# Optimization experiments

Hardware: AMD Instinct MI355X
Metric: run time of the kernel (lower is better)

## Reference

```python
import jax, jax.numpy as jnp
import numpy as np

N_NODES = 50000
N_EDGES = 800000
D_IN = 256
D_OUT = 128
EPS = 1e-9


def setup_inputs() -> dict:
    key = jax.random.key(0)
    ks = jax.random.split(key, 6)
    feat = jax.random.normal(ks[0], (N_NODES, D_IN), dtype=jnp.float32)
    edge_row = jax.random.randint(ks[1], (N_EDGES,), 0, N_NODES)
    edge_col = jax.random.randint(ks[2], (N_EDGES,), 0, N_NODES)
    # normalized adjacency values (positive, ~1/degree scale)
    edge_val = jax.random.uniform(ks[3], (N_EDGES,), dtype=jnp.float32) / 16.0
    # xavier_uniform for Linear(dim_in, dim_out) weights, stored as [D_IN, D_OUT]
    limit = float(np.sqrt(6.0 / (D_IN + D_OUT)))
    W0 = jax.random.uniform(ks[4], (D_IN, D_OUT), minval=-limit, maxval=limit, dtype=jnp.float32)
    W1 = jax.random.uniform(ks[5], (D_IN, D_OUT), minval=-limit, maxval=limit, dtype=jnp.float32)
    zeros = jnp.zeros((D_OUT,), dtype=jnp.float32)
    ones = jnp.ones((D_OUT,), dtype=jnp.float32)
    return {
        "feat": feat,
        "W0": W0, "b0": zeros, "scale0": ones, "offset0": zeros,
        "W1": W1, "b1": zeros, "scale1": ones, "offset1": zeros,
        "edge_row": edge_row, "edge_col": edge_col, "edge_val": edge_val,
    }


def _spmm(edge_row, edge_col, edge_val, x):
    # out[r] += val * x[c] for each edge (r, c, val)  -- sparse adj @ x
    msgs = edge_val[:, None] * x[edge_col]  # [E, D]
    return jax.ops.segment_sum(msgs, edge_row, num_segments=N_NODES)


def _feat_trans(x, W, b, scale, offset):
    h = jax.nn.relu(x @ W + b)  # [N, D_OUT]
    mean = jnp.mean(h, axis=1, keepdims=True)
    var = jnp.var(h, axis=1, keepdims=True) + EPS  # unbiased=False (population var)
    return (h - mean) * scale * jax.lax.rsqrt(var) + offset


def reference(feat, W0, b0, scale0, offset0, W1, b1, scale1, offset1,
              edge_row, edge_col, edge_val):
    # non-first-layer path: feat_hop = [X, A @ X] (order=1), dropout p=0 is identity
    hop1 = _spmm(edge_row, edge_col, edge_val, feat)
    f0 = _feat_trans(feat, W0, b0, scale0, offset0)
    f1 = _feat_trans(hop1, W1, b1, scale1, offset1)
    return jnp.concatenate([f0, f1], axis=1)  # aggr == 'concat'
```

## Files before the change

### kernel.cpp

```cpp
#include <hip/hip_runtime.h>

#define N_NODES 50000
#define N_EDGES 800000
#define D_IN    256
#define D_OUT   128
#define EPS     1e-9f
#define PAD     88

#define SCATTER_BLOCKS 196
#define GEMM_MBLKS     391

#define RPB    128
#define NBUCK  391
#define BCAP   2560

typedef __attribute__((ext_vector_type(8))) short bf16x8;
typedef __attribute__((ext_vector_type(4))) float floatx4;

__device__ __forceinline__ ushort f2bf(float x) {
    unsigned u = __float_as_uint(x);
    u += 0x7fffu + ((u >> 16) & 1u);
    return (ushort)(u >> 16);
}

#define WB_BLOCKS  32
__global__ __launch_bounds__(256) void prep_small(
    const float* __restrict__ W0, const float* __restrict__ W1,
    ushort* __restrict__ Wb, int* __restrict__ gcnt)
{
    int bid = blockIdx.x;
    int t   = threadIdx.x;
    if (bid == 0) {
        for (int i = t; i < NBUCK; i += 256) gcnt[i] = 0;
    } else {
        int g  = (bid - 1) * 256 + t;
        int n  = g >> 5;
        int kq = g & 31;
        const float* W = (n < 128) ? W0 : W1;
        int nn = n & 127;
        union { ushort us[8]; uint4 v; } tmp;
#pragma unroll
        for (int j = 0; j < 8; ++j)
            tmp.us[j] = f2bf(W[(size_t)(kq * 8 + j) * D_OUT + nn]);
        *(uint4*)&Wb[(size_t)n * D_IN + kq * 8] = tmp.v;
    }
}

__global__ __launch_bounds__(256, 3) void gemm_scatter(
    const float* __restrict__ feat, const ushort* __restrict__ Wb,
    const float* __restrict__ bias, const float* __restrict__ scale,
    const float* __restrict__ offset,
    float* __restrict__ out, ushort* __restrict__ Y1,
    const int* __restrict__ er, const int* __restrict__ ec,
    const float* __restrict__ ev, int* __restrict__ gcnt,
    uint2* __restrict__ bedge)
{
    __shared__ ushort As[128 * PAD];
    __shared__ ushort Bs[128 * PAD];

    const int t = threadIdx.x;

    if (blockIdx.x < SCATTER_BLOCKS) {
        int* hist = (int*)As;
        int* base = (int*)Bs;
        for (int i = t; i < NBUCK; i += 256) hist[i] = 0;
        __syncthreads();

        int ebase = blockIdx.x * 4096;
        int   bkt[16], rnk[16];
        uint2 pk[16];
#pragma unroll
        for (int u = 0; u < 16; ++u) {
            int e = ebase + u * 256 + t;
            bool ok = (e < N_EDGES);
            int   r = ok ? er[e] : 0;
            int   c = ok ? ec[e] : 0;
            float v = ok ? ev[e] : 0.f;
            bkt[u] = ok ? (r >> 7) : -1;
            pk[u]  = make_uint2(((unsigned)(r & 127) << 16) | (unsigned)c,
                                __float_as_uint(v));
            if (ok) rnk[u] = atomicAdd(&hist[r >> 7], 1);
        }
        __syncthreads();
        for (int i = t; i < NBUCK; i += 256) {
            int h = hist[i];
            base[i] = h ? atomicAdd(&gcnt[i], h) : 0;
        }
        __syncthreads();
#pragma unroll
        for (int u = 0; u < 16; ++u) {
            if (bkt[u] >= 0) {
                int pos = base[bkt[u]] + rnk[u];
                if (pos < BCAP)
                    bedge[(size_t)bkt[u] * BCAP + pos] = pk[u];
            }
        }
        return;
    }

    const int gbid = blockIdx.x - SCATTER_BLOCKS;
    const int half = gbid / GEMM_MBLKS;
    const int mblk = gbid % GEMM_MBLKS;
    const int wave = t >> 6, lane = t & 63;
    const int quad = lane >> 4, l16 = lane & 15;
    const int m0   = mblk * 128;
    const int n0   = half * 128;

    floatx4 acc[2][8];
#pragma unroll
    for (int mt = 0; mt < 2; ++mt)
#pragma unroll
        for (int nt = 0; nt < 8; ++nt)
            acc[mt][nt] = (floatx4){0.f, 0.f, 0.f, 0.f};

    for (int kt = 0; kt < D_IN; kt += 64) {
#pragma unroll
        for (int i = 0; i < 4; ++i) {
            int g = t + i * 256;
            int row = g >> 3, kq = g & 7;
            int grow = m0 + row;
            union { ushort us[8]; uint4 v; } tmp;
            tmp.v = make_uint4(0u, 0u, 0u, 0u);
            if (grow < N_NODES) {
                const float* p = &feat[(size_t)grow * D_IN + kt + kq * 8];
                float4 v0 = *(const float4*)p;
                float4 v1 = *(const float4*)(p + 4);
                tmp.us[0] = f2bf(v0.x); tmp.us[1] = f2bf(v0.y);
                tmp.us[2] = f2bf(v0.z); tmp.us[3] = f2bf(v0.w);
                tmp.us[4] = f2bf(v1.x); tmp.us[5] = f2bf(v1.y);
                tmp.us[6] = f2bf(v1.z); tmp.us[7] = f2bf(v1.w);
            }
            *(uint4*)&As[row * PAD + kq * 8] = tmp.v;
        }
#pragma unroll
        for (int i = 0; i < 4; ++i) {
            int g = t + i * 256;
            int row = g >> 3, kq = g & 7;
            *(uint4*)&Bs[row * PAD + kq * 8] =
                *(const uint4*)&Wb[(size_t)(n0 + row) * D_IN + kt + kq * 8];
        }
        __syncthreads();

#pragma unroll
        for (int kk = 0; kk < 64; kk += 32) {
            bf16x8 a[2], b[8];
#pragma unroll
            for (int mt = 0; mt < 2; ++mt)
                a[mt] = *(bf16x8*)&As[(wave * 32 + mt * 16 + l16) * PAD + kk + quad * 8];
#pragma unroll
            for (int nt = 0; nt < 8; ++nt)
                b[nt] = *(bf16x8*)&Bs[(nt * 16 + l16) * PAD + kk + quad * 8];
#pragma unroll
            for (int mt = 0; mt < 2; ++mt)
#pragma unroll
                for (int nt = 0; nt < 8; ++nt)
                    acc[mt][nt] = __builtin_amdgcn_mfma_f32_16x16x32_bf16(
                        a[mt], b[nt], acc[mt][nt], 0, 0, 0);
        }
        __syncthreads();
    }

    if (half == 0) {
        float bb[8], sc[8], of[8];
#pragma unroll
        for (int nt = 0; nt < 8; ++nt) {
            bb[nt] = bias[nt * 16 + l16];
            sc[nt] = scale[nt * 16 + l16];
            of[nt] = offset[nt * 16 + l16];
        }
#pragma unroll
        for (int mt = 0; mt < 2; ++mt)
#pragma unroll
            for (int i = 0; i < 4; ++i) {
                float h[8], s = 0.f, q = 0.f;
#pragma unroll
                for (int nt = 0; nt < 8; ++nt) {
                    h[nt] = fmaxf(acc[mt][nt][i] + bb[nt], 0.f);
                    s += h[nt];
                    q += h[nt] * h[nt];
                }
#pragma unroll
                for (int m = 1; m < 16; m <<= 1) {
                    s += __shfl_xor(s, m);
                    q += __shfl_xor(q, m);
                }
                float mean = s * (1.f / 128.f);
                float inv  = rsqrtf(q * (1.f / 128.f) - mean * mean + EPS);
                int row = m0 + wave * 32 + mt * 16 + quad * 4 + i;
                if (row < N_NODES) {
#pragma unroll
                    for (int nt = 0; nt < 8; ++nt)
                        out[(size_t)row * 256 + nt * 16 + l16] =
                            (h[nt] - mean) * sc[nt] * inv + of[nt];
                }
            }
    } else {
#pragma unroll
        for (int mt = 0; mt < 2; ++mt)
#pragma unroll
            for (int i = 0; i < 4; ++i) {
                int row = m0 + wave * 32 + mt * 16 + quad * 4 + i;
                if (row < N_NODES) {
#pragma unroll
                    for (int nt = 0; nt < 8; ++nt)
                        Y1[(size_t)row * D_OUT + nt * 16 + l16] =
                            f2bf(acc[mt][nt][i]);
                }
            }
    }
}

__global__ __launch_bounds__(512) void spmm_gather_ln(
    const int* __restrict__ gcnt, const uint2* __restrict__ bedge,
    const ushort* __restrict__ Y,
    const float* __restrict__ bias, const float* __restrict__ scale,
    const float* __restrict__ offset, float* __restrict__ out)
{
    __shared__ int    cnt[RPB];
    __shared__ int    offx[RPB];
    __shared__ int    pos[RPB];
    __shared__ ushort lcol[BCAP];
    __shared__ float  lval[BCAP];

    const int t      = threadIdx.x;
    const int bucket = blockIdx.x;
    const int r0     = bucket * RPB;
    const int nrows  = min(RPB, N_NODES - r0);
    int ne = gcnt[bucket];
    ne = ne < BCAP ? ne : BCAP;

    if (t < RPB) cnt[t] = 0;
    __syncthreads();
    for (int i = t; i < ne; i += 512) {
        uint2 p = bedge[(size_t)bucket * BCAP + i];
        atomicAdd(&cnt[p.x >> 16], 1);
    }
    __syncthreads();
    if (t < RPB) offx[t] = cnt[t];
    __syncthreads();
    for (int s = 1; s < RPB; s <<= 1) {
        int w = 0;
        if (t < RPB && t >= s) w = offx[t - s];
        __syncthreads();
        if (t < RPB) offx[t] += w;
        __syncthreads();
    }
    if (t < RPB) {
        offx[t] -= cnt[t];
        pos[t]   = offx[t];
    }
    __syncthreads();
    for (int i = t; i < ne; i += 512) {
        uint2 p = bedge[(size_t)bucket * BCAP + i];
        int r = p.x >> 16;
        int k = atomicAdd(&pos[r], 1);
        lcol[k] = (ushort)(p.x & 0xffffu);
        lval[k] = __uint_as_float(p.y);
    }
    __syncthreads();

    const int wave = t >> 6, lane = t & 63;
    const int cidx = lane * 2;
    const float b0v = bias[cidx],   b1v = bias[cidx + 1];
    const float s0v = scale[cidx],  s1v = scale[cidx + 1];
    const float o0v = offset[cidx], o1v = offset[cidx + 1];

    for (int ri = wave; ri < nrows; ri += 8) {
        int beg = offx[ri], n = cnt[ri];
        float ax = 0.f, ay = 0.f;
        int j = 0;
        for (; j + 8 <= n; j += 8) {
            unsigned yv[8]; float vv[8]; int cc[8];
#pragma unroll
            for (int u = 0; u < 8; ++u) {
                cc[u] = lcol[beg + j + u];
                vv[u] = lval[beg + j + u];
                yv[u] = *(const unsigned*)&Y[(size_t)cc[u] * D_OUT + cidx];
            }
#pragma unroll
            for (int u = 0; u < 8; ++u) {
                ax = fmaf(vv[u], __uint_as_float(yv[u] << 16), ax);
                ay = fmaf(vv[u], __uint_as_float(yv[u] & 0xffff0000u), ay);
            }
        }
        for (; j < n; ++j) {
            int   c  = lcol[beg + j];
            float vj = lval[beg + j];
            unsigned yv = *(const unsigned*)&Y[(size_t)c * D_OUT + cidx];
            ax = fmaf(vj, __uint_as_float(yv << 16), ax);
            ay = fmaf(vj, __uint_as_float(yv & 0xffff0000u), ay);
        }
        float h0 = fmaxf(ax + b0v, 0.f);
        float h1 = fmaxf(ay + b1v, 0.f);
        float s = h0 + h1, q = h0 * h0 + h1 * h1;
#pragma unroll
        for (int m = 1; m < 64; m <<= 1) {
            s += __shfl_xor(s, m);
            q += __shfl_xor(q, m);
        }
        float mean = s * (1.f / 128.f);
        float inv  = rsqrtf(q * (1.f / 128.f) - mean * mean + EPS);
        int row = r0 + ri;
        float2 o;
        o.x = (h0 - mean) * s0v * inv + o0v;
        o.y = (h1 - mean) * s1v * inv + o1v;
        *(float2*)&out[(size_t)row * 256 + 128 + cidx] = o;
    }
}

extern "C" void kernel_launch(void* const* d_in, const int* in_sizes, int n_in,
                              void* d_out, int out_size, void* d_ws, size_t ws_size,
                              hipStream_t stream)
{
    const float* feat = (const float*)d_in[0];
    const float* W0   = (const float*)d_in[1];
    const float* b0   = (const float*)d_in[2];
    const float* s0   = (const float*)d_in[3];
    const float* o0   = (const float*)d_in[4];
    const float* W1   = (const float*)d_in[5];
    const float* b1   = (const float*)d_in[6];
    const float* s1   = (const float*)d_in[7];
    const float* o1   = (const float*)d_in[8];
    const int*   er   = (const int*)d_in[9];
    const int*   ec   = (const int*)d_in[10];
    const float* ev   = (const float*)d_in[11];
    float* out = (float*)d_out;

    char*   wsb   = (char*)d_ws;
    ushort* Wb    = (ushort*)(wsb);
    ushort* Y1    = (ushort*)(wsb + 131072);
    int*    gcnt  = (int*)   (wsb + 12931072);
    uint2*  bedge = (uint2*) (wsb + 12932672);

    prep_small<<<1 + WB_BLOCKS, 256, 0, stream>>>(W0, W1, Wb, gcnt);

    gemm_scatter<<<SCATTER_BLOCKS + 2 * GEMM_MBLKS, 256, 0, stream>>>(
        feat, Wb, b0, s0, o0, out, Y1, er, ec, ev, gcnt, bedge);

    spmm_gather_ln<<<NBUCK, 512, 0, stream>>>(
        gcnt, bedge, Y1, b1, s1, o1, out);
}
```

Baseline: 192.7 us.

## Halve bucket size and build per-bucket CSR with register-held edges and wave scan

Edge buckets shrink from 128 to 64 rows, doubling the number of gather blocks, which improves load balance and occupancy in the SpMM+LayerNorm kernel. Each thread now loads up to three edges once into registers and records its atomic rank, so the second global read of the bucket and the second atomic pass are gone. The prefix sum over row counts becomes a single-wave shuffle scan instead of a shared-memory loop with barriers. The new capacity of 1344 per bucket (about 1024 expected edges) still risks silently dropping edges in dense buckets, and the three-edge register design only covers 1536 edges per block, which is enough for that cap.

```diff
diff --git a/kernel.cpp b/kernel.cpp
--- a/kernel.cpp
+++ b/kernel.cpp
@@ -10,9 +10,9 @@
 #define SCATTER_BLOCKS 196
 #define GEMM_MBLKS     391
 
-#define RPB    128
-#define NBUCK  391
-#define BCAP   2560
+#define RPB    64
+#define NBUCK  782
+#define BCAP   1344
 
 typedef __attribute__((ext_vector_type(8))) short bf16x8;
 typedef __attribute__((ext_vector_type(4))) float floatx4;
@@ -76,10 +76,10 @@
             int   r = ok ? er[e] : 0;
             int   c = ok ? ec[e] : 0;
             float v = ok ? ev[e] : 0.f;
-            bkt[u] = ok ? (r >> 7) : -1;
-            pk[u]  = make_uint2(((unsigned)(r & 127) << 16) | (unsigned)c,
+            bkt[u] = ok ? (r >> 6) : -1;
+            pk[u]  = make_uint2(((unsigned)(r & 63) << 16) | (unsigned)c,
                                 __float_as_uint(v));
-            if (ok) rnk[u] = atomicAdd(&hist[r >> 7], 1);
+            if (ok) rnk[u] = atomicAdd(&hist[r >> 6], 1);
         }
         __syncthreads();
         for (int i = t; i < NBUCK; i += 256) {
@@ -210,17 +210,16 @@
     }
 }
 
-__global__ __launch_bounds__(512) void spmm_gather_ln(
+__global__ __launch_bounds__(512) void spmm_csr_ln(
     const int* __restrict__ gcnt, const uint2* __restrict__ bedge,
     const ushort* __restrict__ Y,
     const float* __restrict__ bias, const float* __restrict__ scale,
     const float* __restrict__ offset, float* __restrict__ out)
 {
+    __shared__ ushort lcol[BCAP];
+    __shared__ float  lval[BCAP];
     __shared__ int    cnt[RPB];
     __shared__ int    offx[RPB];
-    __shared__ int    pos[RPB];
-    __shared__ ushort lcol[BCAP];
-    __shared__ float  lval[BCAP];
 
     const int t      = threadIdx.x;
     const int bucket = blockIdx.x;
@@ -231,32 +230,46 @@
 
     if (t < RPB) cnt[t] = 0;
     __syncthreads();
-    for (int i = t; i < ne; i += 512) {
-        uint2 p = bedge[(size_t)bucket * BCAP + i];
-        atomicAdd(&cnt[p.x >> 16], 1);
+
+    const size_t base = (size_t)bucket * BCAP;
+    int   erA = -1, erB = -1, erC = -1;
+    int   ecA = 0,  ecB = 0,  ecC = 0;
+    float evA = 0.f, evB = 0.f, evC = 0.f;
+    int   rkA = 0,  rkB = 0,  rkC = 0;
+    if (t < ne) {
+        uint2 p = bedge[base + t];
+        erA = (int)(p.x >> 16); ecA = (int)(p.x & 0xffffu);
+        evA = __uint_as_float(p.y);
+        rkA = atomicAdd(&cnt[erA], 1);
+    }
+    if (t + 512 < ne) {
+        uint2 p = bedge[base + t + 512];
+        erB = (int)(p.x >> 16); ecB = (int)(p.x & 0xffffu);
+        evB = __uint_as_float(p.y);
+        rkB = atomicAdd(&cnt[erB], 1);
+    }
+    if (t + 1024 < ne) {
+        uint2 p = bedge[base + t + 1024];
+        erC = (int)(p.x >> 16); ecC = (int)(p.x & 0xffffu);
+        evC = __uint_as_float(p.y);
+        rkC = atomicAdd(&cnt[erC], 1);
     }
     __syncthreads();
-    if (t < RPB) offx[t] = cnt[t];
+
+    if (t < RPB) {
+        int c = cnt[t], x = c;
+#pragma unroll
+        for (int s = 1; s < RPB; s <<= 1) {
+            int w = __shfl_up(x, s);
+            if (t >= s) x += w;
+        }
+        offx[t] = x - c;
+    }
     __syncthreads();
-    for (int s = 1; s < RPB; s <<= 1) {
-        int w = 0;
-        if (t < RPB && t >= s) w = offx[t - s];
-        __syncthreads();
-        if (t < RPB) offx[t] += w;
-        __syncthreads();
-    }
-    if (t < RPB) {
-        offx[t] -= cnt[t];
-        pos[t]   = offx[t];
-    }
-    __syncthreads();
-    for (int i = t; i < ne; i += 512) {
-        uint2 p = bedge[(size_t)bucket * BCAP + i];
-        int r = p.x >> 16;
-        int k = atomicAdd(&pos[r], 1);
-        lcol[k] = (ushort)(p.x & 0xffffu);
-        lval[k] = __uint_as_float(p.y);
-    }
+
+    if (erA >= 0) { int k = offx[erA] + rkA; lcol[k] = (ushort)ecA; lval[k] = evA; }
+    if (erB >= 0) { int k = offx[erB] + rkB; lcol[k] = (ushort)ecB; lval[k] = evB; }
+    if (erC >= 0) { int k = offx[erC] + rkC; lcol[k] = (ushort)ecC; lval[k] = evC; }
     __syncthreads();
 
     const int wave = t >> 6, lane = t & 63;
@@ -330,13 +343,13 @@
     ushort* Wb    = (ushort*)(wsb);
     ushort* Y1    = (ushort*)(wsb + 131072);
     int*    gcnt  = (int*)   (wsb + 12931072);
-    uint2*  bedge = (uint2*) (wsb + 12932672);
+    uint2*  bedge = (uint2*) (wsb + 12935168);
 
     prep_small<<<1 + WB_BLOCKS, 256, 0, stream>>>(W0, W1, Wb, gcnt);
 
     gemm_scatter<<<SCATTER_BLOCKS + 2 * GEMM_MBLKS, 256, 0, stream>>>(
         feat, Wb, b0, s0, o0, out, Y1, er, ec, ev, gcnt, bedge);
 
-    spmm_gather_ln<<<NBUCK, 512, 0, stream>>>(
+    spmm_csr_ln<<<NBUCK, 512, 0, stream>>>(
         gcnt, bedge, Y1, b1, s1, o1, out);
 }
```

Measured after the change: 179.2 us. 1.08x faster.
